# Kernel optimization log

Hardware: AMD Instinct MI355X
Metric: run time of the kernel (lower is better)

## Reference

```python
import jax, jax.numpy as jnp
import numpy as np

B, T, V, E, H, M, O = 256, 512, 32000, 512, 1024, 1024, 2


def _xavier(key, shape):
    fan_out, fan_in = shape[0], shape[1]
    std = (2.0 / (fan_in + fan_out)) ** 0.5
    return (jax.random.normal(key, shape) * std).astype(jnp.float32)


def setup_inputs() -> dict:
    key = jax.random.key(0)
    ks = jax.random.split(key, 13)
    inv_sqrt_h = 1.0 / np.sqrt(H)
    inp = {
        "x": jax.random.randint(ks[0], (B, T), 0, V),
        "x_index": jax.random.randint(ks[1], (B,), 0, T),
        "emb_table": jax.random.normal(ks[2], (V + 1, E), dtype=jnp.float32),
        # LSTMCell params (torch layout: W_ih [4H,E], W_hh [4H,H], gate order i,f,g,o)
        "W_ih": (jax.random.uniform(ks[3], (4 * H, E), minval=-1.0, maxval=1.0) * inv_sqrt_h).astype(jnp.float32),
        "W_hh": (jax.random.uniform(ks[4], (4 * H, H), minval=-1.0, maxval=1.0) * inv_sqrt_h).astype(jnp.float32),
        "b_ih": (jax.random.uniform(ks[5], (4 * H,), minval=-1.0, maxval=1.0) * inv_sqrt_h).astype(jnp.float32),
        "b_hh": (jax.random.uniform(ks[6], (4 * H,), minval=-1.0, maxval=1.0) * inv_sqrt_h).astype(jnp.float32),
        # MLP params
        "fc1_w": _xavier(ks[7], (M, H)),
        "fc1_b": jnp.zeros((M,), jnp.float32),
        "fc2_w": _xavier(ks[8], (O, M)),
        "fc2_b": jnp.zeros((O,), jnp.float32),
        # torch code xavier-normal-inits h0/c0 each forward; made explicit here
        "h0": _xavier(ks[9], (B, H)),
        "c0": _xavier(ks[10], (B, H)),
    }
    return inp


def reference(x, x_index, emb_table, W_ih, W_hh, b_ih, b_hh,
              fc1_w, fc1_b, fc2_w, fc2_b, h0, c0):
    emb = emb_table[x]  # [B,T,E]
    # precompute input-to-gate projection for all timesteps in one GEMM
    xg = jnp.einsum('bte,ge->btg', emb, W_ih) + b_ih + b_hh  # [B,T,4H]

    def step(carry, xg_t):
        h, c = carry
        gates = xg_t + h @ W_hh.T  # [B,4H]
        i, f, g, o = jnp.split(gates, 4, axis=-1)
        i = jax.nn.sigmoid(i)
        f = jax.nn.sigmoid(f)
        g = jnp.tanh(g)
        o = jax.nn.sigmoid(o)
        c = f * c + i * g
        h = o * jnp.tanh(c)
        return (h, c), h

    (_, _), out = jax.lax.scan(step, (h0, c0), jnp.swapaxes(xg, 0, 1))
    out = jnp.swapaxes(out, 0, 1)  # [B,T,H]
    hn = out[jnp.arange(out.shape[0]), x_index]  # [B,H] hidden at last valid pos
    z = jnp.tanh(hn @ fc1_w.T + fc1_b)
    logits = z @ fc2_w.T + fc2_b
    return jax.nn.log_softmax(logits, axis=-1)
```

## Files before the change

kernel.cpp:

```cpp
#include <hip/hip_runtime.h>

typedef unsigned short u16;
typedef unsigned int u32;
typedef unsigned long long u64;
typedef __attribute__((ext_vector_type(8))) short short8;
typedef __attribute__((ext_vector_type(4))) float floatx4;
typedef __attribute__((ext_vector_type(4))) u32 u32x4;

#define B_   256
#define T_   512
#define E_   512
#define H_   1024
#define G4H  4096
#define KCAT 1536
#define M_   1024

#define RG_N    8
#define RG_ROWS 32
#define CB_N    32
#define HC_B    32
#define NW      8
#define AL_STRIDE 1544

__device__ __forceinline__ u16 f2bf(float f) {
    union { float f; unsigned u; } v; v.f = f;
    unsigned r = (v.u + 0x7fffu + ((v.u >> 16) & 1u)) >> 16;
    return (u16)r;
}
__device__ __forceinline__ float sigf(float x) {
    return __fdividef(1.0f, 1.0f + __expf(-x));
}
__device__ __forceinline__ float tanh_f(float x) {
    return 1.0f - __fdividef(2.0f, __expf(2.0f * x) + 1.0f);
}


__global__ void sort_rows(const int* __restrict__ x_index,
                          int* __restrict__ perm, int* __restrict__ sxi) {
    __shared__ int xl[B_];
    int tid = threadIdx.x;
    xl[tid] = x_index[tid];
    __syncthreads();
    int mine = xl[tid], rank = 0;
    for (int j = 0; j < B_; ++j)
        rank += (xl[j] > mine) || (xl[j] == mine && j < tid);
    perm[rank] = tid;
    sxi[rank] = mine;
}

__global__ void prep_emb(const int* __restrict__ x, const float* __restrict__ tab,
                         const int* __restrict__ perm, u16* __restrict__ emb) {
    int idx = (blockIdx.x * 256 + threadIdx.x) * 4;
    int srow = idx >> 18;
    int t    = (idx >> 9) & 511;
    int e    = idx & 511;
    int orig = perm[srow];
    int xv   = x[orig * T_ + t];
    float4 v = *(const float4*)(tab + (size_t)xv * E_ + e);
    ushort4 o; o.x = f2bf(v.x); o.y = f2bf(v.y); o.z = f2bf(v.z); o.w = f2bf(v.w);
    *(ushort4*)(emb + idx) = o;
}

__global__ void prep_wcat(const float* __restrict__ Whh, const float* __restrict__ Wih,
                          u16* __restrict__ wcat) {
    int idx = (blockIdx.x * 256 + threadIdx.x) * 4;
    int g = idx / KCAT;
    int k = idx - g * KCAT;
    const float* src = (k < H_) ? (Whh + (size_t)g * H_ + k)
                                : (Wih + (size_t)g * E_ + (k - H_));
    float4 v = *(const float4*)src;
    ushort4 o; o.x = f2bf(v.x); o.y = f2bf(v.y); o.z = f2bf(v.z); o.w = f2bf(v.w);
    *(ushort4*)(wcat + idx) = o;
}

__global__ void prep_fc1w(const float* __restrict__ src, u16* __restrict__ dst) {
    int idx = (blockIdx.x * 256 + threadIdx.x) * 4;
    float4 v = *(const float4*)(src + idx);
    ushort4 o; o.x = f2bf(v.x); o.y = f2bf(v.y); o.z = f2bf(v.z); o.w = f2bf(v.w);
    *(ushort4*)(dst + idx) = o;
}

__global__ void prep_bias(const float* __restrict__ bih, const float* __restrict__ bhh,
                          float* __restrict__ bias) {
    int i = blockIdx.x * 256 + threadIdx.x;
    bias[i] = bih[i] + bhh[i];
}

__global__ void prep_state(const float* __restrict__ h0, const float* __restrict__ c0,
                           const int* __restrict__ perm,
                           u16* __restrict__ hbuf0, float* __restrict__ c0p) {
    int i = blockIdx.x * 256 + threadIdx.x;
    int srow = i >> 10, col = i & 1023;
    int orig = perm[srow];
    hbuf0[i] = f2bf(h0[(size_t)orig * H_ + col]);
    c0p[i]   = c0[(size_t)orig * H_ + col];
}

__global__ void zero_flags(u32* __restrict__ f) {
    f[blockIdx.x * 256 + threadIdx.x] = 0;
}


__global__ __launch_bounds__(512, 2) void lstm_persist(
    const u16* __restrict__ emb, const u16* __restrict__ wcat,
    const float* __restrict__ bias, const float* __restrict__ c0p,
    const int* __restrict__ sxi,
    u16* __restrict__ hbuf, float* __restrict__ hn, u32* __restrict__ flags)
{
    __shared__ __align__(16) u16 Albuf[32 * AL_STRIDE];
    __shared__ __align__(16) float Gf_all[NW][640];

    const int tid  = threadIdx.x;
    const int w    = tid >> 6;
    const int lane = tid & 63;
    const int lr   = lane & 15;
    const int lk   = lane >> 4;
    const int rg   = blockIdx.x >> 5;
    const int cb   = blockIdx.x & 31;

    const int gc = (lr & 3) * H_ + cb * HC_B + w * 4 + (lr >> 2);
    const u16* wrow = wcat + (size_t)gc * KCAT + lk * 8;
    short8 Breg[48];
    #pragma unroll
    for (int ks = 0; ks < 48; ++ks)
        Breg[ks] = *(const short8*)(wrow + ks * 32);

    const int r0    = lane >> 1;
    const int hp    = lane & 1;
    const int hcol0 = cb * HC_B + w * 4 + hp * 2;
    const int rowg  = rg * RG_ROWS + r0;
    const int tmax  = sxi[rg * RG_ROWS];
    const int xi    = sxi[rowg];
    float2 cc = *(const float2*)(c0p + (size_t)rowg * H_ + hcol0);
    const float2 bI = *(const float2*)(bias + 0 * H_ + hcol0);
    const float2 bF = *(const float2*)(bias + 1 * H_ + hcol0);
    const float2 bG = *(const float2*)(bias + 2 * H_ + hcol0);
    const float2 bO = *(const float2*)(bias + 3 * H_ + hcol0);

    const u32* fp = flags + rg * CB_N;

    const size_t hrow_u16 = (size_t)(rg * RG_ROWS + w * 4) * H_;
    const int    erow_l   = w * 4 + (lane >> 4);
    const u16*   erow_p   = emb + (size_t)(rg * RG_ROWS + erow_l) * T_ * E_;
    const int    echunk   = (lane & 15) * 8;

    for (int t = 0; t <= tmax; ++t) {
        const u16* hread  = hbuf + (size_t)(t & 1) * (B_ * H_);
        u16*       hwrite = hbuf + (size_t)((t + 1) & 1) * (B_ * H_);

        if (t > 0) {
            while (true) {
                u32 v = (lane < 32)
                    ? __hip_atomic_load(fp + lane, __ATOMIC_RELAXED,
                                        __HIP_MEMORY_SCOPE_AGENT)
                    : (u32)t;
                if (__all((int)(v >= (u32)t))) break;
                __builtin_amdgcn_s_sleep(1);
            }
        }

        {
            u64* hsrc = (u64*)(hread + hrow_u16);
            #pragma unroll
            for (int b = 0; b < 2; ++b) {
                u64 htmp[8];
                #pragma unroll
                for (int i = 0; i < 8; ++i)
                    htmp[i] = __hip_atomic_load(hsrc + (b * 8 + i) * 64 + lane,
                                                __ATOMIC_RELAXED,
                                                __HIP_MEMORY_SCOPE_AGENT);
                #pragma unroll
                for (int i = 0; i < 8; ++i) {
                    int hb = (b * 8 + i) * 512 + lane * 8;
                    *(u64*)&Albuf[(w * 4 + (hb >> 11)) * AL_STRIDE + ((hb & 2047) >> 1)] = htmp[i];
                }
            }
        }
        {
            const u16* esrc = erow_p + (size_t)t * E_ + echunk;
            u32x4 etmp[4];
            #pragma unroll
            for (int i = 0; i < 4; ++i)
                etmp[i] = *(const u32x4*)(esrc + i * 128);
            #pragma unroll
            for (int i = 0; i < 4; ++i)
                *(u32x4*)&Albuf[erow_l * AL_STRIDE + 1024 + echunk + i * 128] = etmp[i];
        }

        __syncthreads();

        floatx4 acc00 = {0,0,0,0}, acc01 = {0,0,0,0};
        floatx4 acc10 = {0,0,0,0}, acc11 = {0,0,0,0};
        #pragma unroll
        for (int ks = 0; ks < 48; ++ks) {
            short8 a0 = *(const short8*)&Albuf[lr * AL_STRIDE + ks * 32 + lk * 8];
            short8 a1 = *(const short8*)&Albuf[(16 + lr) * AL_STRIDE + ks * 32 + lk * 8];
            if (ks & 1) {
                acc01 = __builtin_amdgcn_mfma_f32_16x16x32_bf16(a0, Breg[ks], acc01, 0, 0, 0);
                acc11 = __builtin_amdgcn_mfma_f32_16x16x32_bf16(a1, Breg[ks], acc11, 0, 0, 0);
            } else {
                acc00 = __builtin_amdgcn_mfma_f32_16x16x32_bf16(a0, Breg[ks], acc00, 0, 0, 0);
                acc10 = __builtin_amdgcn_mfma_f32_16x16x32_bf16(a1, Breg[ks], acc10, 0, 0, 0);
            }
        }

        float* Gf = Gf_all[w];
        #pragma unroll
        for (int r = 0; r < 4; ++r) {
            Gf[(lk * 4 + r) * 20 + lr]        = acc00[r] + acc01[r];
            Gf[(16 + lk * 4 + r) * 20 + lr]   = acc10[r] + acc11[r];
        }
        float4 gA = *(float4*)&Gf[r0 * 20 + hp * 8];
        float4 gB = *(float4*)&Gf[r0 * 20 + hp * 8 + 4];

        float i0 = sigf(gA.x + bI.x), f0 = sigf(gA.y + bF.x);
        float q0 = tanh_f(gA.z + bG.x), o0 = sigf(gA.w + bO.x);
        float i1 = sigf(gB.x + bI.y), f1 = sigf(gB.y + bF.y);
        float q1 = tanh_f(gB.z + bG.y), o1 = sigf(gB.w + bO.y);
        cc.x = f0 * cc.x + i0 * q0;
        cc.y = f1 * cc.y + i1 * q1;
        float h0f = o0 * tanh_f(cc.x);
        float h1f = o1 * tanh_f(cc.y);

        u32 packed = (u32)f2bf(h0f) | ((u32)f2bf(h1f) << 16);
        __hip_atomic_store((u32*)(hwrite + (size_t)rowg * H_ + hcol0), packed,
                           __ATOMIC_RELAXED, __HIP_MEMORY_SCOPE_AGENT);
        if (xi == t)
            *(float2*)(hn + (size_t)rowg * H_ + hcol0) = make_float2(h0f, h1f);

        __syncthreads();
        if (tid == 0)
            __hip_atomic_store(flags + rg * CB_N + cb, (u32)(t + 1),
                               __ATOMIC_RELAXED, __HIP_MEMORY_SCOPE_AGENT);
    }
}


__global__ void hn_convert(const float* __restrict__ hn, u16* __restrict__ hnbf) {
    int i = blockIdx.x * 256 + threadIdx.x;
    hnbf[i] = f2bf(hn[i]);
}

__global__ __launch_bounds__(256) void fc1_kernel(
    const u16* __restrict__ A, const u16* __restrict__ Bw,
    const float* __restrict__ bvec, float* __restrict__ z)
{
    __shared__ __align__(16) u16 Als[64 * 72];
    __shared__ __align__(16) u16 Bls[64 * 72];
    const int tid = threadIdx.x;
    const int rowbase = blockIdx.y * 64;
    const int colbase = blockIdx.x * 64;
    floatx4 acc[4] = {{0,0,0,0},{0,0,0,0},{0,0,0,0},{0,0,0,0}};
    const int w = tid >> 6, lane = tid & 63, lr = lane & 15, lk = lane >> 4;

    for (int s = 0; s < H_ / 64; ++s) {
        int k0 = s * 64;
        #pragma unroll
        for (int cc2 = 0; cc2 < 2; ++cc2) {
            int c = tid + cc2 * 256;
            int row = c >> 3, kg = c & 7, kglob = k0 + kg * 8;
            *(u32x4*)&Als[(row * 9 + kg) * 8] =
                *(const u32x4*)(A + (size_t)(rowbase + row) * H_ + kglob);
            *(u32x4*)&Bls[(row * 9 + kg) * 8] =
                *(const u32x4*)(Bw + (size_t)(colbase + row) * H_ + kglob);
        }
        __syncthreads();
        #pragma unroll
        for (int ks = 0; ks < 2; ++ks) {
            short8 a = *(const short8*)&Als[((16 * w + lr) * 9 + ks * 4 + lk) * 8];
            #pragma unroll
            for (int q = 0; q < 4; ++q) {
                short8 b = *(const short8*)&Bls[((q * 16 + lr) * 9 + ks * 4 + lk) * 8];
                acc[q] = __builtin_amdgcn_mfma_f32_16x16x32_bf16(a, b, acc[q], 0, 0, 0);
            }
        }
        __syncthreads();
    }
    #pragma unroll
    for (int q = 0; q < 4; ++q) {
        int col = colbase + q * 16 + lr;
        float bb = bvec[col];
        #pragma unroll
        for (int r = 0; r < 4; ++r) {
            int row = rowbase + 16 * w + lk * 4 + r;
            z[(size_t)row * M_ + col] = tanh_f(acc[q][r] + bb);
        }
    }
}

__global__ __launch_bounds__(64) void fc2_softmax(
    const float* __restrict__ z, const float* __restrict__ wmat,
    const float* __restrict__ bvec, const int* __restrict__ perm,
    float* __restrict__ out)
{
    int bi = blockIdx.x;
    int lane = threadIdx.x;
    const float4* zr = (const float4*)(z + (size_t)bi * M_);
    const float4* w0 = (const float4*)(wmat);
    const float4* w1 = (const float4*)(wmat + M_);
    float s0 = 0.f, s1 = 0.f;
    for (int k = lane; k < M_ / 4; k += 64) {
        float4 zv = zr[k]; float4 a = w0[k]; float4 c = w1[k];
        s0 += zv.x * a.x + zv.y * a.y + zv.z * a.z + zv.w * a.w;
        s1 += zv.x * c.x + zv.y * c.y + zv.z * c.z + zv.w * c.w;
    }
    for (int off = 32; off; off >>= 1) {
        s0 += __shfl_down(s0, off);
        s1 += __shfl_down(s1, off);
    }
    if (lane == 0) {
        float l0 = s0 + bvec[0], l1 = s1 + bvec[1];
        float m = fmaxf(l0, l1);
        float lse = m + __logf(__expf(l0 - m) + __expf(l1 - m));
        int orig = perm[bi];
        out[orig * 2 + 0] = l0 - lse;
        out[orig * 2 + 1] = l1 - lse;
    }
}


extern "C" void kernel_launch(void* const* d_in, const int* in_sizes, int n_in,
                              void* d_out, int out_size, void* d_ws, size_t ws_size,
                              hipStream_t stream)
{
    const int*   x       = (const int*)  d_in[0];
    const int*   x_index = (const int*)  d_in[1];
    const float* emb_t   = (const float*)d_in[2];
    const float* W_ih    = (const float*)d_in[3];
    const float* W_hh    = (const float*)d_in[4];
    const float* b_ih    = (const float*)d_in[5];
    const float* b_hh    = (const float*)d_in[6];
    const float* fc1_w   = (const float*)d_in[7];
    const float* fc1_b   = (const float*)d_in[8];
    const float* fc2_w   = (const float*)d_in[9];
    const float* fc2_b   = (const float*)d_in[10];
    const float* h0      = (const float*)d_in[11];
    const float* c0      = (const float*)d_in[12];
    float* out = (float*)d_out;

    char* p = (char*)d_ws;
    u16*   emb_bf = (u16*)p;   p += (size_t)B_ * T_ * E_ * 2;
    u16*   wcat   = (u16*)p;   p += (size_t)G4H * KCAT * 2;
    u16*   fc1wbf = (u16*)p;   p += (size_t)M_ * H_ * 2;
    float* bias   = (float*)p; p += (size_t)G4H * 4;
    u16*   hbuf   = (u16*)p;   p += (size_t)2 * B_ * H_ * 2;
    float* c0p    = (float*)p; p += (size_t)B_ * H_ * 4;
    float* hn     = (float*)p; p += (size_t)B_ * H_ * 4;
    u16*   hnbf   = (u16*)p;   p += (size_t)B_ * H_ * 2;
    float* zbuf   = (float*)p; p += (size_t)B_ * M_ * 4;
    int*   perm   = (int*)p;   p += (size_t)B_ * 4;
    int*   sxi    = (int*)p;   p += (size_t)B_ * 4;
    u32*   flags  = (u32*)p;   p += (size_t)16 * 128 * 4;

    sort_rows <<<1,     256, 0, stream>>>(x_index, perm, sxi);
    prep_emb  <<<65536, 256, 0, stream>>>(x, emb_t, perm, emb_bf);
    prep_wcat <<<6144,  256, 0, stream>>>(W_hh, W_ih, wcat);
    prep_fc1w <<<1024,  256, 0, stream>>>(fc1_w, fc1wbf);
    prep_bias <<<16,    256, 0, stream>>>(b_ih, b_hh, bias);
    prep_state<<<1024,  256, 0, stream>>>(h0, c0, perm, hbuf, c0p);
    zero_flags<<<8,     256, 0, stream>>>(flags);

    lstm_persist<<<256, 512, 0, stream>>>(emb_bf, wcat, bias, c0p, sxi,
                                          hbuf, hn, flags);

    hn_convert <<<1024, 256, 0, stream>>>(hn, hnbf);
    fc1_kernel <<<dim3(16, 4), 256, 0, stream>>>(hnbf, fc1wbf, fc1_b, zbuf);
    fc2_softmax<<<256, 64, 0, stream>>>(zbuf, fc2_w, fc2_b, perm, out);
}
```

Measured before the change: 3.615 ms.

## Overlap embedding-projection MFMAs with flag wait via double-buffered embedding LDS

```diff
diff --git a/kernel.cpp b/kernel.cpp
--- a/kernel.cpp
+++ b/kernel.cpp
@@ -20,7 +20,8 @@
 #define CB_N    32
 #define HC_B    32
 #define NW      8
-#define AL_STRIDE 1544
+#define HSTRIDE 1032
+#define ESTRIDE 520
 
 __device__ __forceinline__ u16 f2bf(float f) {
     union { float f; unsigned u; } v; v.f = f;
@@ -107,7 +108,8 @@
     const int* __restrict__ sxi,
     u16* __restrict__ hbuf, float* __restrict__ hn, u32* __restrict__ flags)
 {
-    __shared__ __align__(16) u16 Albuf[32 * AL_STRIDE];
+    __shared__ __align__(16) u16 Hl[32 * HSTRIDE];
+    __shared__ __align__(16) u16 El[2 * 32 * ESTRIDE];
     __shared__ __align__(16) float Gf_all[NW][640];
 
     const int tid  = threadIdx.x;
@@ -125,6 +127,8 @@
     for (int ks = 0; ks < 48; ++ks)
         Breg[ks] = *(const short8*)(wrow + ks * 32);
 
+    const float biasv = bias[gc];
+
     const int r0    = lane >> 1;
     const int hp    = lane & 1;
     const int hcol0 = cb * HC_B + w * 4 + hp * 2;
@@ -132,10 +136,6 @@
     const int tmax  = sxi[rg * RG_ROWS];
     const int xi    = sxi[rowg];
     float2 cc = *(const float2*)(c0p + (size_t)rowg * H_ + hcol0);
-    const float2 bI = *(const float2*)(bias + 0 * H_ + hcol0);
-    const float2 bF = *(const float2*)(bias + 1 * H_ + hcol0);
-    const float2 bG = *(const float2*)(bias + 2 * H_ + hcol0);
-    const float2 bO = *(const float2*)(bias + 3 * H_ + hcol0);
 
     const u32* fp = flags + rg * CB_N;
 
@@ -144,9 +144,40 @@
     const u16*   erow_p   = emb + (size_t)(rg * RG_ROWS + erow_l) * T_ * E_;
     const int    echunk   = (lane & 15) * 8;
 
+    {
+        const u16* esrc = erow_p + echunk;
+        u32x4 etmp[4];
+        #pragma unroll
+        for (int i = 0; i < 4; ++i)
+            etmp[i] = *(const u32x4*)(esrc + i * 128);
+        #pragma unroll
+        for (int i = 0; i < 4; ++i)
+            *(u32x4*)&El[erow_l * ESTRIDE + echunk + i * 128] = etmp[i];
+    }
+    __syncthreads();
+
     for (int t = 0; t <= tmax; ++t) {
         const u16* hread  = hbuf + (size_t)(t & 1) * (B_ * H_);
         u16*       hwrite = hbuf + (size_t)((t + 1) & 1) * (B_ * H_);
+
+        floatx4 acc00 = {biasv, biasv, biasv, biasv}, acc01 = {0,0,0,0};
+        floatx4 acc10 = {biasv, biasv, biasv, biasv}, acc11 = {0,0,0,0};
+
+        {
+            const int eb = (t & 1) * (32 * ESTRIDE);
+            #pragma unroll
+            for (int ks2 = 0; ks2 < 16; ++ks2) {
+                short8 a0 = *(const short8*)&El[eb + lr * ESTRIDE + ks2 * 32 + lk * 8];
+                short8 a1 = *(const short8*)&El[eb + (16 + lr) * ESTRIDE + ks2 * 32 + lk * 8];
+                if (ks2 & 1) {
+                    acc01 = __builtin_amdgcn_mfma_f32_16x16x32_bf16(a0, Breg[32 + ks2], acc01, 0, 0, 0);
+                    acc11 = __builtin_amdgcn_mfma_f32_16x16x32_bf16(a1, Breg[32 + ks2], acc11, 0, 0, 0);
+                } else {
+                    acc00 = __builtin_amdgcn_mfma_f32_16x16x32_bf16(a0, Breg[32 + ks2], acc00, 0, 0, 0);
+                    acc10 = __builtin_amdgcn_mfma_f32_16x16x32_bf16(a1, Breg[32 + ks2], acc10, 0, 0, 0);
+                }
+            }
+        }
 
         if (t > 0) {
             while (true) {
@@ -172,29 +203,29 @@
                 #pragma unroll
                 for (int i = 0; i < 8; ++i) {
                     int hb = (b * 8 + i) * 512 + lane * 8;
-                    *(u64*)&Albuf[(w * 4 + (hb >> 11)) * AL_STRIDE + ((hb & 2047) >> 1)] = htmp[i];
+                    *(u64*)&Hl[(w * 4 + (hb >> 11)) * HSTRIDE + ((hb & 2047) >> 1)] = htmp[i];
                 }
             }
         }
-        {
-            const u16* esrc = erow_p + (size_t)t * E_ + echunk;
+
+        __syncthreads();
+
+        if (t < tmax) {
+            const u16* esrc = erow_p + (size_t)(t + 1) * E_ + echunk;
             u32x4 etmp[4];
             #pragma unroll
             for (int i = 0; i < 4; ++i)
                 etmp[i] = *(const u32x4*)(esrc + i * 128);
+            const int eb2 = ((t + 1) & 1) * (32 * ESTRIDE);
             #pragma unroll
             for (int i = 0; i < 4; ++i)
-                *(u32x4*)&Albuf[erow_l * AL_STRIDE + 1024 + echunk + i * 128] = etmp[i];
-        }
-
-        __syncthreads();
-
-        floatx4 acc00 = {0,0,0,0}, acc01 = {0,0,0,0};
-        floatx4 acc10 = {0,0,0,0}, acc11 = {0,0,0,0};
-        #pragma unroll
-        for (int ks = 0; ks < 48; ++ks) {
-            short8 a0 = *(const short8*)&Albuf[lr * AL_STRIDE + ks * 32 + lk * 8];
-            short8 a1 = *(const short8*)&Albuf[(16 + lr) * AL_STRIDE + ks * 32 + lk * 8];
+                *(u32x4*)&El[eb2 + erow_l * ESTRIDE + echunk + i * 128] = etmp[i];
+        }
+
+        #pragma unroll
+        for (int ks = 0; ks < 32; ++ks) {
+            short8 a0 = *(const short8*)&Hl[lr * HSTRIDE + ks * 32 + lk * 8];
+            short8 a1 = *(const short8*)&Hl[(16 + lr) * HSTRIDE + ks * 32 + lk * 8];
             if (ks & 1) {
                 acc01 = __builtin_amdgcn_mfma_f32_16x16x32_bf16(a0, Breg[ks], acc01, 0, 0, 0);
                 acc11 = __builtin_amdgcn_mfma_f32_16x16x32_bf16(a1, Breg[ks], acc11, 0, 0, 0);
@@ -207,16 +238,16 @@
         float* Gf = Gf_all[w];
         #pragma unroll
         for (int r = 0; r < 4; ++r) {
-            Gf[(lk * 4 + r) * 20 + lr]        = acc00[r] + acc01[r];
-            Gf[(16 + lk * 4 + r) * 20 + lr]   = acc10[r] + acc11[r];
+            Gf[(lk * 4 + r) * 20 + lr]      = acc00[r] + acc01[r];
+            Gf[(16 + lk * 4 + r) * 20 + lr] = acc10[r] + acc11[r];
         }
         float4 gA = *(float4*)&Gf[r0 * 20 + hp * 8];
         float4 gB = *(float4*)&Gf[r0 * 20 + hp * 8 + 4];
 
-        float i0 = sigf(gA.x + bI.x), f0 = sigf(gA.y + bF.x);
-        float q0 = tanh_f(gA.z + bG.x), o0 = sigf(gA.w + bO.x);
-        float i1 = sigf(gB.x + bI.y), f1 = sigf(gB.y + bF.y);
-        float q1 = tanh_f(gB.z + bG.y), o1 = sigf(gB.w + bO.y);
+        float i0 = sigf(gA.x), f0 = sigf(gA.y);
+        float q0 = tanh_f(gA.z), o0 = sigf(gA.w);
+        float i1 = sigf(gB.x), f1 = sigf(gB.y);
+        float q1 = tanh_f(gB.z), o1 = sigf(gB.w);
         cc.x = f0 * cc.x + i0 * q0;
         cc.y = f1 * cc.y + i1 * q1;
         float h0f = o0 * tanh_f(cc.x);
```

Result: faster. 2.958 ms (-18.2%).
